# Kernel tuning notes

Hardware: AMD Instinct MI355X
Metric: run time of the kernel (lower is better)

The kernel has to match this reference:

```python
import jax, jax.numpy as jnp
import numpy as np

N, E, K_ORDER = 50000, 800000, 3
F_IN, H = 128, 128


def setup_inputs() -> dict:
    key = jax.random.key(0)
    ks = jax.random.split(key, 24)
    s = 0.05
    inp = {
        "x_t": jax.random.normal(ks[0], (N, F_IN), jnp.float32),
        "h_prev": jax.random.normal(ks[1], (N, H), jnp.float32),
        "c_prev": jax.random.normal(ks[2], (N, H), jnp.float32),
        "edge_weight": jax.random.uniform(ks[3], (E,), jnp.float32),
        "edge_index": jax.random.randint(ks[4], (2, E), 0, N, dtype=jnp.int64),
    }
    # Input->gate weight matrices W_* : (F, H)
    for i, nm in enumerate(["W_i", "W_f", "W_c", "W_o"]):
        inp[nm] = jax.random.normal(ks[5 + i], (F_IN, H), jnp.float32) * s
    # ChebConv weights theta_* : (K, H, H) applied to hidden state
    for i, nm in enumerate(["theta_i", "theta_f", "theta_c", "theta_o"]):
        inp[nm] = jax.random.normal(ks[9 + i], (K_ORDER, H, H), jnp.float32) * s
    # Gate biases (b_* of GCLSTM merged with the ChebConv bias; they add)
    for i, nm in enumerate(["b_i", "b_f", "b_c", "b_o"]):
        inp[nm] = jax.random.normal(ks[13 + i], (H,), jnp.float32) * s
    # Peephole weights w_c_* : (H,)
    for i, nm in enumerate(["w_ci", "w_cf", "w_co"]):
        inp[nm] = jax.random.normal(ks[17 + i], (H,), jnp.float32) * s
    return inp


def _cheb_norm(edge_index, edge_weight):
    # get_laplacian('sym') + lambda_max=2 scaling + add_self_loops(-1)
    # => L~ = -D^{-1/2} A D^{-1/2}  (zero diagonal)
    src, dst = edge_index[0], edge_index[1]
    deg = jax.ops.segment_sum(edge_weight, src, num_segments=N)
    dinv = jnp.where(deg > 0, jax.lax.rsqrt(jnp.maximum(deg, 1e-30)), 0.0)
    return src, dst, -edge_weight * dinv[src] * dinv[dst]


def _cheb_conv(x, theta, bias, src, dst, wn):
    # Chebyshev recursion: Tx0=x, Tx1=L~x, Tx_k = 2 L~ Tx_{k-1} - Tx_{k-2}
    def Lmul(v):
        return jax.ops.segment_sum(wn[:, None] * v[src], dst, num_segments=N)
    Tx0 = x
    Tx1 = Lmul(x)
    out = Tx0 @ theta[0] + Tx1 @ theta[1]
    for k in range(2, theta.shape[0]):
        Tx2 = 2.0 * Lmul(Tx1) - Tx0
        out = out + Tx2 @ theta[k]
        Tx0, Tx1 = Tx1, Tx2
    return out + bias


def reference(x_t, h_prev, c_prev, edge_weight, W_i, W_f, W_c, W_o,
              theta_i, theta_f, theta_c, theta_o, b_i, b_f, b_c, b_o,
              w_ci, w_cf, w_co, edge_index):
    src, dst, wn = _cheb_norm(edge_index, edge_weight)
    i = jax.nn.sigmoid(x_t @ W_i + _cheb_conv(h_prev, theta_i, b_i, src, dst, wn)
                       + w_ci * c_prev)
    f = jax.nn.sigmoid(x_t @ W_f + _cheb_conv(h_prev, theta_f, b_f, src, dst, wn)
                       + w_cf * c_prev)
    t = jnp.tanh(x_t @ W_c + _cheb_conv(h_prev, theta_c, b_c, src, dst, wn))
    c_t = f * c_prev + i * t
    o = jax.nn.sigmoid(x_t @ W_o + _cheb_conv(h_prev, theta_o, b_o, src, dst, wn)
                       + w_co * c_t)
    h_t = o * jnp.tanh(c_t)
    return (h_t, c_t)
```

## Files before the change

kernel.cpp:

```cpp
#include <hip/hip_runtime.h>

#define NN 50000
#define EE 800000
#define KC 64
#define EPC (EE / KC)
#define DEG_SCALE 4096.0f

typedef float f32x4 __attribute__((ext_vector_type(4)));
typedef short bf16x8 __attribute__((ext_vector_type(8)));
typedef unsigned short u16x8 __attribute__((ext_vector_type(8)));

__device__ __forceinline__ unsigned short f2bf(float f) {
  unsigned int u = __float_as_uint(f);
  u += 0x7fffu + ((u >> 16) & 1u);
  return (unsigned short)(u >> 16);
}
__device__ __forceinline__ float bf2f(unsigned short u) {
  return __uint_as_float(((unsigned int)u) << 16);
}

__device__ __forceinline__ void async_copy16(const void* g, void* l) {
  __builtin_amdgcn_global_load_lds(
      (const __attribute__((address_space(1))) unsigned int*)g,
      (__attribute__((address_space(3))) unsigned int*)l, 16, 0, 0);
}

__device__ __forceinline__ float fast_sig(float x) {
  return __builtin_amdgcn_rcpf(1.f + __expf(-x));
}
__device__ __forceinline__ float fast_tanh(float x) {
  return 1.f - 2.f * __builtin_amdgcn_rcpf(__expf(2.f * x) + 1.f);
}

__device__ __forceinline__ unsigned short* hslot2(char* o, long j) {
  return (unsigned short*)(o + (j >> 7) * 512 + (j & 127) * 2);
}
__device__ __forceinline__ void store8u16(char* o, long s, uint4 v) {
  *(uint4*)(o + (s >> 7) * 512 + (s & 127) * 2) = v;
}
#define CNT_SLOT0 3200000L
#define RANK_SLOT0 3200000L

__global__ __launch_bounds__(1024) void k_pre(
    const float* __restrict__ Wi, const float* __restrict__ Wf,
    const float* __restrict__ Wc, const float* __restrict__ Wo,
    const float* __restrict__ Ti, const float* __restrict__ Tf,
    const float* __restrict__ Tc, const float* __restrict__ To,
    unsigned short* __restrict__ bglob, const float* __restrict__ h,
    const float* __restrict__ x, char* __restrict__ outB,
    const int* __restrict__ src, const int* __restrict__ dst,
    const float* __restrict__ w) {
  __shared__ unsigned hist[25000];
  const int b = blockIdx.x, tid = threadIdx.x;
  char* cB = outB + (long)NN * 512;
  if (b < KC) {
    uint4* h4 = (uint4*)hist;
    const int base = b * EPC;
    for (int j = tid; j < 6250; j += 1024) h4[j] = (uint4){0u, 0u, 0u, 0u};
    __syncthreads();
    for (int k = tid; k < EPC; k += 1024) {
      const int e = base + k;
      const int d = dst[e];
      const int sh = (d & 1) * 16;
      const unsigned old = atomicAdd(&hist[d >> 1], 1u << sh);
      *hslot2(cB, RANK_SLOT0 + e) = (unsigned short)((old >> sh) & 0xffffu);
    }
    __syncthreads();
    for (int j = tid; j < 6250; j += 1024)
      store8u16(outB, CNT_SLOT0 + (long)b * NN + j * 8, h4[j]);
    __syncthreads();
    for (int j = tid; j < 6250; j += 1024) h4[j] = (uint4){0u, 0u, 0u, 0u};
    __syncthreads();
    for (int k = tid; k < EPC; k += 1024) {
      const int e = base + k;
      const int s = src[e];
      const unsigned q = (unsigned)__float2uint_rn(w[e] * DEG_SCALE);
      const int sh = (s & 1) * 16;
      atomicAdd(&hist[s >> 1], q << sh);
    }
    __syncthreads();
    for (int j = tid; j < 6250; j += 1024)
      store8u16(outB, (long)b * NN + j * 8, h4[j]);
  } else if (b < KC + 32) {
    const int t = (b - KC) * 1024 + tid;
    const int ks = t >> 11;
    const int cf = (t >> 6) & 31;
    const int lane = t & 63;
    const int wv = cf >> 3, hl = (cf >> 2) & 1, g = cf & 3;
    const int kg = lane >> 4, lm = lane & 15;
    const int hc = (wv * 2 + hl) * 16 + lm;
    const float* Wg = (g == 0) ? Wi : (g == 1) ? Wf : (g == 2) ? Wc : Wo;
    const float* Tg = (g == 0) ? Ti : (g == 1) ? Tf : (g == 2) ? Tc : To;
    u16x8 out;
#pragma unroll
    for (int dk = 0; dk < 8; ++dk) {
      const int k = ks * 32 + kg * 8 + dk;
      const int kb = k >> 7, r = k & 127;
      const float v = (kb == 0) ? Wg[r * 128 + hc] : Tg[(kb - 1) * 16384 + r * 128 + hc];
      out[dk] = f2bf(v);
    }
    *(u16x8*)(bglob + t * 8) = out;
  } else if (b < KC + 32 + 782) {
    const int i = (b - (KC + 32)) * 1024 + tid;
    if (i < 100000 * 8) {
      const float* hp = h + i * 8;
      const f32x4 v0 = *(const f32x4*)hp;
      const f32x4 v1 = *(const f32x4*)(hp + 4);
      u16x8 o;
#pragma unroll
      for (int e = 0; e < 4; ++e) o[e] = f2bf(v0[e]);
#pragma unroll
      for (int e = 0; e < 4; ++e) o[e + 4] = f2bf(v1[e]);
      *(u16x8*)(outB + (i >> 4) * 512 + 256 + (i & 15) * 16) = o;
    }
  } else {
    const int i = (b - (KC + 32 + 782)) * 1024 + tid;
    if (i < 100000 * 8) {
      const float* xp = x + i * 8;
      const f32x4 v0 = *(const f32x4*)xp;
      const f32x4 v1 = *(const f32x4*)(xp + 4);
      u16x8 o;
#pragma unroll
      for (int e = 0; e < 4; ++e) o[e] = f2bf(v0[e]);
#pragma unroll
      for (int e = 0; e < 4; ++e) o[e + 4] = f2bf(v1[e]);
      *(u16x8*)(cB + (i >> 4) * 512 + 256 + (i & 15) * 16) = o;
    }
  }
}

__device__ __forceinline__ int block_scan_excl_256(int v, int* total) {
  __shared__ int wsum[4];
  const int tid = threadIdx.x;
  const int lane = tid & 63, wv = tid >> 6;
  int x = v;
#pragma unroll
  for (int d = 1; d < 64; d <<= 1) {
    const int y = __shfl_up(x, d, 64);
    if (lane >= d) x += y;
  }
  if (lane == 63) wsum[wv] = x;
  __syncthreads();
  int pre = 0, tot = 0;
#pragma unroll
  for (int u = 0; u < 4; ++u) {
    const int s = wsum[u];
    pre += (u < wv) ? s : 0;
    tot += s;
  }
  *total = tot;
  return pre + x - v;
}

__global__ void k_phase2(char* __restrict__ outB, float* __restrict__ dinv,
                         int* __restrict__ wscnt, int* __restrict__ bsum) {
  char* cB = outB + (long)NN * 512;
  const int i = blockIdx.x * 256 + threadIdx.x;
  int run = 0;
  if (i < NN) {
    float s = 0.f;
#pragma unroll
    for (int c = 0; c < KC; ++c)
      s += (float)*hslot2(outB, (long)c * NN + i);
    s *= (1.0f / DEG_SCALE);
    dinv[i] = (s > 0.f) ? rsqrtf(fmaxf(s, 1e-30f)) : 0.f;
#pragma unroll
    for (int c = 0; c < KC; ++c) {
      *hslot2(cB, (long)c * NN + i) = (unsigned short)run;
      run += (int)*hslot2(outB, CNT_SLOT0 + (long)c * NN + i);
    }
    wscnt[i] = run;
  }
  int tot;
  block_scan_excl_256(run, &tot);
  if (threadIdx.x == 0) bsum[blockIdx.x] = tot;
}

__global__ void k_scan2(const int* __restrict__ bsum, int* __restrict__ boff,
                        const int nb) {
  const int t = threadIdx.x;
  const int v = (t < nb) ? bsum[t] : 0;
  int tot;
  const int excl = block_scan_excl_256(v, &tot);
  if (t <= nb) boff[t] = excl;
}

__global__ void k_scan3(const int* __restrict__ cnt, const int* __restrict__ boff,
                        int* __restrict__ off) {
  const int i = blockIdx.x * 256 + threadIdx.x;
  const int v = (i < NN) ? cnt[i] : 0;
  int tot;
  const int excl = block_scan_excl_256(v, &tot) + boff[blockIdx.x];
  if (i < NN) off[i] = excl;
  if (i == NN) off[NN] = excl;
}

__global__ void k_edge2(const int* __restrict__ src, const int* __restrict__ dst,
                        const float* __restrict__ w, const float* __restrict__ dinv,
                        const int* __restrict__ off, char* __restrict__ outB,
                        int2* __restrict__ ed) {
  const int e = blockIdx.x * blockDim.x + threadIdx.x;
  if (e >= EE) return;
  char* cB = outB + (long)NN * 512;
  const int s = src[e], d = dst[e];
  const int c = e / EPC;
  const int p = off[d] + (int)*hslot2(cB, (long)c * NN + d) +
                (int)*hslot2(cB, RANK_SLOT0 + e);
  int2 rec;
  rec.x = s;
  rec.y = __float_as_int(-w[e] * dinv[s] * dinv[d]);
  ed[p] = rec;
}

__global__ __launch_bounds__(256) void k_gather(
    const char* __restrict__ vinB, const char* __restrict__ vsubB, const float alpha,
    const int* __restrict__ off, const int2* __restrict__ ed, char* __restrict__ voutB) {
  const int wid = threadIdx.x >> 6, lane = threadIdx.x & 63;
  const int node = blockIdx.x * 4 + wid;
  const int p0 = off[node], p1 = off[node + 1];
  const int lb = lane * 4;
  float ax0 = 0.f, ay0 = 0.f, ax1 = 0.f, ay1 = 0.f;
  float ax2 = 0.f, ay2 = 0.f, ax3 = 0.f, ay3 = 0.f;
  int p = p0;
  for (; p + 7 < p1; p += 8) {
    int2 E[8];
    unsigned V[8];
#pragma unroll
    for (int u = 0; u < 8; ++u) E[u] = ed[p + u];
#pragma unroll
    for (int u = 0; u < 8; ++u)
      V[u] = *(const unsigned*)(vinB + (long)E[u].x * 512 + lb);
#pragma unroll
    for (int u = 0; u < 8; ++u) {
      const float wv = __int_as_float(E[u].y);
      float* ax = (u & 3) == 0 ? &ax0 : (u & 3) == 1 ? &ax1 : (u & 3) == 2 ? &ax2 : &ax3;
      float* ay = (u & 3) == 0 ? &ay0 : (u & 3) == 1 ? &ay1 : (u & 3) == 2 ? &ay2 : &ay3;
      *ax = fmaf(wv, bf2f((unsigned short)V[u]), *ax);
      *ay = fmaf(wv, bf2f((unsigned short)(V[u] >> 16)), *ay);
    }
  }
  for (; p + 3 < p1; p += 4) {
    const int2 e0 = ed[p], e1 = ed[p + 1], e2 = ed[p + 2], e3 = ed[p + 3];
    const unsigned v0 = *(const unsigned*)(vinB + (long)e0.x * 512 + lb);
    const unsigned v1 = *(const unsigned*)(vinB + (long)e1.x * 512 + lb);
    const unsigned v2 = *(const unsigned*)(vinB + (long)e2.x * 512 + lb);
    const unsigned v3 = *(const unsigned*)(vinB + (long)e3.x * 512 + lb);
    const float w0 = __int_as_float(e0.y), w1 = __int_as_float(e1.y);
    const float w2 = __int_as_float(e2.y), w3 = __int_as_float(e3.y);
    ax0 = fmaf(w0, bf2f((unsigned short)v0), ax0);
    ay0 = fmaf(w0, bf2f((unsigned short)(v0 >> 16)), ay0);
    ax1 = fmaf(w1, bf2f((unsigned short)v1), ax1);
    ay1 = fmaf(w1, bf2f((unsigned short)(v1 >> 16)), ay1);
    ax2 = fmaf(w2, bf2f((unsigned short)v2), ax2);
    ay2 = fmaf(w2, bf2f((unsigned short)(v2 >> 16)), ay2);
    ax3 = fmaf(w3, bf2f((unsigned short)v3), ax3);
    ay3 = fmaf(w3, bf2f((unsigned short)(v3 >> 16)), ay3);
  }
  for (; p < p1; ++p) {
    const int2 e0 = ed[p];
    const unsigned v0 = *(const unsigned*)(vinB + (long)e0.x * 512 + lb);
    const float w0 = __int_as_float(e0.y);
    ax0 = fmaf(w0, bf2f((unsigned short)v0), ax0);
    ay0 = fmaf(w0, bf2f((unsigned short)(v0 >> 16)), ay0);
  }
  float rx = alpha * ((ax0 + ax1) + (ax2 + ax3));
  float ry = alpha * ((ay0 + ay1) + (ay2 + ay3));
  if (vsubB) {
    const unsigned s = *(const unsigned*)(vsubB + (long)node * 512 + lb);
    rx -= bf2f((unsigned short)s);
    ry -= bf2f((unsigned short)(s >> 16));
  }
  const unsigned ow = (unsigned)f2bf(rx) | ((unsigned)f2bf(ry) << 16);
  *(unsigned*)(voutB + (long)node * 512 + lb) = ow;
}

__global__ __launch_bounds__(512, 4) void k_gemm(
    const char* __restrict__ outB, const unsigned short* __restrict__ bglob,
    const float* __restrict__ c_prev,
    const float* __restrict__ b_i, const float* __restrict__ b_f,
    const float* __restrict__ b_c, const float* __restrict__ b_o,
    const float* __restrict__ w_ci, const float* __restrict__ w_cf,
    const float* __restrict__ w_co, float* __restrict__ h_out,
    float* __restrict__ c_out) {
  __shared__ char lds[65536];
  const int tid = threadIdx.x;
  const int lane = tid & 63;
  const int w = tid >> 6;
  const int kg = lane >> 4;
  const int lm = lane & 15;
  const int m0 = blockIdx.x * 64;

  const char* hB = outB;
  const char* cB = outB + (long)NN * 512;

  {
    const int t8 = tid & 255;
    const int rf = t8 >> 6, ln = t8 & 63;
    const int srow0 = m0 + rf * 16 + (ln & 15);
    const long srow = (srow0 < NN) ? srow0 : (NN - 1);
    const int schunk = (ln >> 4) * 16;
#pragma unroll
    for (int i = 0; i < 8; ++i) {
      const int ks = i * 2 + (tid >> 8);
      const char* base = (ks < 4) ? (cB + 256) : (ks < 8) ? (hB + 256) : (ks < 12) ? hB : cB;
      async_copy16(base + srow * 512 + (ks & 3) * 64 + schunk,
                   &lds[ks * 4096 + t8 * 16]);
    }
  }

  f32x4 acc[16];
#pragma unroll
  for (int i = 0; i < 16; ++i) acc[i] = (f32x4){0.f, 0.f, 0.f, 0.f};

  bf16x8 b0[4], b1[4];
  auto loadB = [&](int ks, bf16x8* bb) {
    const unsigned short* fp = bglob + ((ks * 32 + w * 4) * 64 + lane) * 8;
#pragma unroll
    for (int g = 0; g < 4; ++g) bb[g] = *(const bf16x8*)(fp + g * 512);
  };

  __syncthreads();

  loadB(0, b0);
#pragma unroll
  for (int ks = 0; ks < 16; ++ks) {
    bf16x8* bc = (ks & 1) ? b1 : b0;
    bf16x8* bn = (ks & 1) ? b0 : b1;
    if (ks < 15) loadB(ks + 1, bn);
    bf16x8 a[4];
#pragma unroll
    for (int rf = 0; rf < 4; ++rf)
      a[rf] = *(const bf16x8*)(&lds[ks * 4096 + rf * 1024 + lane * 16]);
#pragma unroll
    for (int rf = 0; rf < 4; ++rf)
#pragma unroll
      for (int g = 0; g < 4; ++g)
        acc[rf * 4 + g] =
            __builtin_amdgcn_mfma_f32_16x16x32_bf16(a[rf], bc[g], acc[rf * 4 + g], 0, 0, 0);
  }

  const int hc = w * 16 + lm;
  const float bi = b_i[hc], bfv = b_f[hc], bc_ = b_c[hc], bo = b_o[hc];
  const float wci = w_ci[hc], wcf = w_cf[hc], wco = w_co[hc];
#pragma unroll
  for (int rf = 0; rf < 4; ++rf) {
#pragma unroll
    for (int reg = 0; reg < 4; ++reg) {
      const int node = m0 + rf * 16 + kg * 4 + reg;
      if (node < NN) {
        const float cp = c_prev[node * 128 + hc];
        const float pi = acc[rf * 4 + 0][reg] + bi + wci * cp;
        const float pf = acc[rf * 4 + 1][reg] + bfv + wcf * cp;
        const float pc = acc[rf * 4 + 2][reg] + bc_;
        const float po = acc[rf * 4 + 3][reg] + bo;
        const float ig = fast_sig(pi);
        const float fg = fast_sig(pf);
        const float ct = fg * cp + ig * fast_tanh(pc);
        const float og = fast_sig(po + wco * ct);
        h_out[node * 128 + hc] = og * fast_tanh(ct);
        c_out[node * 128 + hc] = ct;
      }
    }
  }
}


extern "C" void kernel_launch(void* const* d_in, const int* in_sizes, int n_in,
                              void* d_out, int out_size, void* d_ws, size_t ws_size,
                              hipStream_t stream) {
  const float* x_t    = (const float*)d_in[0];
  const float* h_prev = (const float*)d_in[1];
  const float* c_prev = (const float*)d_in[2];
  const float* ew     = (const float*)d_in[3];
  const int*   eidx   = (const int*)d_in[4];
  const float* Wi = (const float*)d_in[5];
  const float* Wf = (const float*)d_in[6];
  const float* Wc = (const float*)d_in[7];
  const float* Wo = (const float*)d_in[8];
  const float* Ti = (const float*)d_in[9];
  const float* Tf = (const float*)d_in[10];
  const float* Tc = (const float*)d_in[11];
  const float* To = (const float*)d_in[12];
  const float* bi = (const float*)d_in[13];
  const float* bf = (const float*)d_in[14];
  const float* bc = (const float*)d_in[15];
  const float* bo = (const float*)d_in[16];
  const float* wci = (const float*)d_in[17];
  const float* wcf = (const float*)d_in[18];
  const float* wco = (const float*)d_in[19];

  char* ws = (char*)d_ws;
  float* dinv  = (float*)(ws + 0);
  int*   wscnt = (int*)(ws + 200192);
  int*   off   = (int*)(ws + 400384);
  int*   bsum  = (int*)(ws + 601088);
  int*   boff  = (int*)(ws + 602112);
  int2*  ed    = (int2*)(ws + 603136);
  unsigned short* bglob = (unsigned short*)(ws + 7003136);

  char* outB = (char*)d_out;
  float* h_out = (float*)d_out;
  float* c_out = h_out + (long)NN * 128;

  const int* esrc = eidx;
  const int* edst = eidx + EE;

  k_pre<<<KC + 32 + 782 + 782, 1024, 0, stream>>>(
      Wi, Wf, Wc, Wo, Ti, Tf, Tc, To, bglob, h_prev, x_t, outB, esrc, edst, ew);
  k_phase2<<<196, 256, 0, stream>>>(outB, dinv, wscnt, bsum);
  k_scan2<<<1, 256, 0, stream>>>(bsum, boff, 196);
  k_scan3<<<196, 256, 0, stream>>>(wscnt, boff, off);
  k_edge2<<<3125, 256, 0, stream>>>(esrc, edst, ew, dinv, off, outB, ed);
  k_gather<<<12500, 256, 0, stream>>>(outB + 256, nullptr, 1.f, off, ed, outB);
  k_gather<<<12500, 256, 0, stream>>>(outB, outB + 256, 2.f, off, ed,
                                      outB + (long)NN * 512);
  k_gemm<<<782, 512, 0, stream>>>(outB, bglob, c_prev,
                                  bi, bf, bc, bo, wci, wcf, wco, h_out, c_out);
}
```

Baseline: 210.3 us.

## Parallelize per-node chunk scan across a wavefront and deepen GEMM B prefetch

Phase2 previously had one thread per node loop serially over 64 chunks, using only 196 blocks. It now assigns one wavefront per node, with a lane per chunk, and does the exclusive prefix via shuffles and the degree sum via an xor reduction. The block-sum step moves into a separate k_scan1 kernel. The GEMM B-operand register pipeline goes from double buffering to a triple buffer prefetched three steps ahead, to hide global-load latency at the cost of more VGPRs and one extra kernel launch.

```diff
diff --git a/kernel.cpp b/kernel.cpp
--- a/kernel.cpp
+++ b/kernel.cpp
@@ -129,6 +129,32 @@
   }
 }
 
+__global__ __launch_bounds__(256) void k_phase2(char* __restrict__ outB,
+                                                float* __restrict__ dinv,
+                                                int* __restrict__ wscnt) {
+  char* cB = outB + (long)NN * 512;
+  const int lane = threadIdx.x & 63;
+  const int i = blockIdx.x * 4 + (threadIdx.x >> 6);
+  const int c = lane;
+  const int cnt_c = (int)*hslot2(outB, CNT_SLOT0 + (long)c * NN + i);
+  const float deg_c = (float)*hslot2(outB, (long)c * NN + i);
+  int x = cnt_c;
+#pragma unroll
+  for (int d = 1; d < 64; d <<= 1) {
+    const int y = __shfl_up(x, d, 64);
+    if (lane >= d) x += y;
+  }
+  *hslot2(cB, (long)c * NN + i) = (unsigned short)(x - cnt_c);
+  float s = deg_c;
+#pragma unroll
+  for (int d = 1; d < 64; d <<= 1) s += __shfl_xor(s, d, 64);
+  if (lane == 0) {
+    s *= (1.0f / DEG_SCALE);
+    dinv[i] = (s > 0.f) ? rsqrtf(fmaxf(s, 1e-30f)) : 0.f;
+  }
+  if (lane == 63) wscnt[i] = x;
+}
+
 __device__ __forceinline__ int block_scan_excl_256(int v, int* total) {
   __shared__ int wsum[4];
   const int tid = threadIdx.x;
@@ -152,27 +178,11 @@
   return pre + x - v;
 }
 
-__global__ void k_phase2(char* __restrict__ outB, float* __restrict__ dinv,
-                         int* __restrict__ wscnt, int* __restrict__ bsum) {
-  char* cB = outB + (long)NN * 512;
+__global__ void k_scan1(const int* __restrict__ wscnt, int* __restrict__ bsum) {
   const int i = blockIdx.x * 256 + threadIdx.x;
-  int run = 0;
-  if (i < NN) {
-    float s = 0.f;
-#pragma unroll
-    for (int c = 0; c < KC; ++c)
-      s += (float)*hslot2(outB, (long)c * NN + i);
-    s *= (1.0f / DEG_SCALE);
-    dinv[i] = (s > 0.f) ? rsqrtf(fmaxf(s, 1e-30f)) : 0.f;
-#pragma unroll
-    for (int c = 0; c < KC; ++c) {
-      *hslot2(cB, (long)c * NN + i) = (unsigned short)run;
-      run += (int)*hslot2(outB, CNT_SLOT0 + (long)c * NN + i);
-    }
-    wscnt[i] = run;
-  }
+  const int v = (i < NN) ? wscnt[i] : 0;
   int tot;
-  block_scan_excl_256(run, &tot);
+  block_scan_excl_256(v, &tot);
   if (threadIdx.x == 0) bsum[blockIdx.x] = tot;
 }
 
@@ -312,21 +322,22 @@
 #pragma unroll
   for (int i = 0; i < 16; ++i) acc[i] = (f32x4){0.f, 0.f, 0.f, 0.f};
 
-  bf16x8 b0[4], b1[4];
+  bf16x8 B[3][4];
   auto loadB = [&](int ks, bf16x8* bb) {
     const unsigned short* fp = bglob + ((ks * 32 + w * 4) * 64 + lane) * 8;
 #pragma unroll
     for (int g = 0; g < 4; ++g) bb[g] = *(const bf16x8*)(fp + g * 512);
   };
 
+  loadB(0, B[0]);
+  loadB(1, B[1]);
+  loadB(2, B[2]);
+
   __syncthreads();
 
-  loadB(0, b0);
 #pragma unroll
   for (int ks = 0; ks < 16; ++ks) {
-    bf16x8* bc = (ks & 1) ? b1 : b0;
-    bf16x8* bn = (ks & 1) ? b0 : b1;
-    if (ks < 15) loadB(ks + 1, bn);
+    const int m = ks % 3;
     bf16x8 a[4];
 #pragma unroll
     for (int rf = 0; rf < 4; ++rf)
@@ -336,7 +347,8 @@
 #pragma unroll
       for (int g = 0; g < 4; ++g)
         acc[rf * 4 + g] =
-            __builtin_amdgcn_mfma_f32_16x16x32_bf16(a[rf], bc[g], acc[rf * 4 + g], 0, 0, 0);
+            __builtin_amdgcn_mfma_f32_16x16x32_bf16(a[rf], B[m][g], acc[rf * 4 + g], 0, 0, 0);
+    if (ks + 3 < 16) loadB(ks + 3, B[m]);
   }
 
   const int hc = w * 16 + lm;
@@ -407,7 +419,8 @@
 
   k_pre<<<KC + 32 + 782 + 782, 1024, 0, stream>>>(
       Wi, Wf, Wc, Wo, Ti, Tf, Tc, To, bglob, h_prev, x_t, outB, esrc, edst, ew);
-  k_phase2<<<196, 256, 0, stream>>>(outB, dinv, wscnt, bsum);
+  k_phase2<<<12500, 256, 0, stream>>>(outB, dinv, wscnt);
+  k_scan1<<<196, 256, 0, stream>>>(wscnt, bsum);
   k_scan2<<<1, 256, 0, stream>>>(bsum, boff, 196);
   k_scan3<<<196, 256, 0, stream>>>(wscnt, boff, off);
   k_edge2<<<3125, 256, 0, stream>>>(esrc, edst, ew, dinv, off, outB, ed);
```

After: 197.2 us. 1.07x faster.
